# Optimization experiments

Hardware: AMD Instinct MI355X
Metric: run time of the kernel (lower is better)

The kernel has to match this reference:

```python
import jax, jax.numpy as jnp
import numpy as np

B, H, S, D = 2, 16, 2048, 64

def setup_inputs() -> dict:
    key = jax.random.key(0)
    kq, kk, kv, km = jax.random.split(key, 4)
    Q = jax.random.normal(kq, (B, H, S, D), dtype=jnp.float32)
    K = jax.random.normal(kk, (B, H, S, D), dtype=jnp.float32)
    V = jax.random.normal(kv, (B, H, S, D), dtype=jnp.float32)
    attn_mask = jax.random.bernoulli(km, 0.5, (B, H, S, S))  # True = masked
    return {"Q": Q, "K": K, "V": V, "attn_mask": attn_mask}

def reference(Q, K, V, attn_mask):
    eps = 1e-12
    d_tensor = K.shape[-1]
    # scores: [B, H, S, S]
    scores = jnp.einsum('bhqd,bhkd->bhqk', Q, K) / np.sqrt(d_tensor).astype(jnp.float32)
    # Faithful to source: first fill mask==0 positions with -eps, then mask==True with -1e9.
    scores = jnp.where(attn_mask == 0, jnp.float32(-eps), scores)
    scores = jnp.where(attn_mask, jnp.float32(-1e9), scores)
    attn = jax.nn.softmax(scores, axis=-1)
    context = jnp.einsum('bhqk,bhkd->bhqd', attn, V)
    # dropout=0.0 (eval) -> identity
    return (context, attn)
```

## Files before the change

kernel.cpp:

```cpp
#include <hip/hip_runtime.h>
#include <hip/hip_bf16.h>
#include <stdint.h>

#define S 2048
#define D 64
#define BH 32
#define NROWS (BH * S)
#define CTX_ELEMS (NROWS * D)
#define NVTB 512
#define VT_BYTES ((size_t)BH * 64 * 64 * 32 * 2)

typedef __attribute__((ext_vector_type(8))) __bf16 bf16x8;
typedef __attribute__((ext_vector_type(4))) float f32x4;
typedef __attribute__((ext_vector_type(4))) int   i32x4;


__global__ __launch_bounds__(256) void k_mask(const int* __restrict__ mask,
                                              const float* __restrict__ V,
                                              float* __restrict__ attn,
                                              uint32_t* __restrict__ packed,
                                              __bf16* __restrict__ VT,
                                              int use_vt) {
  const int t = threadIdx.x;

  if (blockIdx.x < NVTB) {
    if (!use_vt) return;
    const int bh = blockIdx.x >> 4;
    const int kk0 = (blockIdx.x & 15) * 4;
    const int c = t >> 2;
    const int g = t & 3;
#pragma unroll
    for (int s = 0; s < 4; ++s) {
      const int kk = kk0 + s;
      const float* vp = V + ((long)bh * S + kk * 32 + g * 8) * D + c;
      bf16x8 o;
#pragma unroll
      for (int j = 0; j < 8; ++j) o[j] = (__bf16)vp[(long)j * D];
      *reinterpret_cast<bf16x8*>(VT + (((long)bh * 64 + kk) * 64 + c) * 32 + g * 8) = o;
    }
    return;
  }

  const int r = blockIdx.x - NVTB;
  const long base = (long)r * S + t * 8;

  const i32x4 m0 = __builtin_nontemporal_load((const i32x4*)(mask + base));
  const i32x4 m1 = __builtin_nontemporal_load((const i32x4*)(mask + base + 4));
  int v[8] = {m0[0], m0[1], m0[2], m0[3], m1[0], m1[1], m1[2], m1[3]};

  unsigned byte = 0;
  int cnt = 0;
#pragma unroll
  for (int j = 0; j < 8; ++j) {
    unsigned u = (v[j] == 0) ? 1u : 0u;
    byte |= u << j;
    cnt += (int)u;
  }
#pragma unroll
  for (int off = 32; off > 0; off >>= 1) cnt += __shfl_down(cnt, off, 64);

  __shared__ int wsum[4];
  __shared__ unsigned char bts[256];
  bts[t] = (unsigned char)byte;
  if ((t & 63) == 0) wsum[t >> 6] = cnt;
  __syncthreads();

  const int total = wsum[0] + wsum[1] + wsum[2] + wsum[3];
  const float inv = (total > 0) ? (1.0f / (float)total) : 0.0f;

  f32x4 a0, a1;
  a0[0] = (byte & 1u)   ? inv : 0.0f;
  a0[1] = (byte & 2u)   ? inv : 0.0f;
  a0[2] = (byte & 4u)   ? inv : 0.0f;
  a0[3] = (byte & 8u)   ? inv : 0.0f;
  a1[0] = (byte & 16u)  ? inv : 0.0f;
  a1[1] = (byte & 32u)  ? inv : 0.0f;
  a1[2] = (byte & 64u)  ? inv : 0.0f;
  a1[3] = (byte & 128u) ? inv : 0.0f;
  __builtin_nontemporal_store(a0, (f32x4*)(attn + base));
  __builtin_nontemporal_store(a1, (f32x4*)(attn + base + 4));

  if (t < 64) {
    uint32_t w = (uint32_t)bts[4 * t]
               | ((uint32_t)bts[4 * t + 1] << 8)
               | ((uint32_t)bts[4 * t + 2] << 16)
               | ((uint32_t)bts[4 * t + 3] << 24);
    packed[(long)r * 64 + t] = w;
  }
}

#define BMC 128
template<bool USE_VT>
__global__ __launch_bounds__(128) void k_ctx(const uint32_t* __restrict__ packed,
                                             const float* __restrict__ V,
                                             const __bf16* __restrict__ VT,
                                             float* __restrict__ ctx) {
  const int flat = blockIdx.x;
  const int wid = (flat & 7) * ((NROWS / BMC) / 8) + (flat >> 3);
  const int qt = wid & 15;
  const int bh = wid >> 4;

  const int t = threadIdx.x;
  const int lane = t & 63;
  const int w = t >> 6;
  const int l15 = lane & 15;
  const int lk = lane >> 4;

  __shared__ uint32_t pk[BMC * 65];
  __shared__ float invs[BMC];

  const long R0 = (long)bh * S + (long)qt * BMC;

  for (int i = t; i < BMC * 64; i += 128)
    pk[(i >> 6) * 65 + (i & 63)] = packed[(R0 + (i >> 6)) * 64 + (i & 63)];
  __syncthreads();

  {
    int c = 0;
#pragma unroll
    for (int i = 0; i < 64; ++i) c += __popc(pk[t * 65 + i]);
    invs[t] = (c > 0) ? (1.0f / (float)c) : 0.0f;
  }
  __syncthreads();

  const uint8_t* pkb = (const uint8_t*)pk;
  const uint8_t* ap[4];
#pragma unroll
  for (int mt = 0; mt < 4; ++mt)
    ap[mt] = pkb + (w * 64 + mt * 16 + l15) * 260 + lk;
  const __bf16* vt0 = VT + ((long)bh * 64) * 64 * 32 + (long)l15 * 32 + lk * 8;
  const float* vf0 = V + (long)bh * S * D + (long)lk * 8 * D + l15;

  f32x4 acc[4][4];
#pragma unroll
  for (int a = 0; a < 4; ++a)
#pragma unroll
    for (int b = 0; b < 4; ++b) acc[a][b] = f32x4{0.f, 0.f, 0.f, 0.f};

  auto LOADB = [&](bf16x8* dst, uint32_t* by, int kk) {
    if (USE_VT) {
#pragma unroll
      for (int n4 = 0; n4 < 4; ++n4)
        dst[n4] = *reinterpret_cast<const bf16x8*>(vt0 + ((long)kk * 64 + n4 * 16) * 32);
    } else {
      const float* vp = vf0 + (long)kk * 32 * D;
#pragma unroll
      for (int n4 = 0; n4 < 4; ++n4) {
        bf16x8 x;
#pragma unroll
        for (int j = 0; j < 8; ++j) x[j] = (__bf16)vp[j * D + n4 * 16];
        dst[n4] = x;
      }
    }
#pragma unroll
    for (int mt = 0; mt < 4; ++mt) by[mt] = ap[mt][kk * 4];
  };

  auto COMPUTE = [&](const bf16x8* bf, const uint32_t* by) {
#pragma unroll
    for (int mt = 0; mt < 4; ++mt) {
      union { uint32_t u[4]; bf16x8 v; } am;
#pragma unroll
      for (int p = 0; p < 4; ++p) {
        am.u[p] = (((by[mt] >> (2 * p)) & 1u) ? 0x3F80u : 0u)
                | (((by[mt] >> (2 * p + 1)) & 1u) ? 0x3F800000u : 0u);
      }
#pragma unroll
      for (int n4 = 0; n4 < 4; ++n4)
        acc[mt][n4] = __builtin_amdgcn_mfma_f32_16x16x32_bf16(am.v, bf[n4], acc[mt][n4], 0, 0, 0);
    }
  };

  bf16x8 bA[4], bB[4];
  uint32_t byA[4], byB[4];
  LOADB(bA, byA, 0);
#pragma unroll 1
  for (int kk = 0; kk < S / 32; kk += 2) {
    LOADB(bB, byB, kk + 1);
    COMPUTE(bA, byA);
    if (kk + 2 < S / 32) LOADB(bA, byA, kk + 2);
    COMPUTE(bB, byB);
  }

#pragma unroll
  for (int mt = 0; mt < 4; ++mt) {
#pragma unroll
    for (int ri = 0; ri < 4; ++ri) {
      const int rloc = w * 64 + mt * 16 + lk * 4 + ri;
      const float iv = invs[rloc];
      const long orow = R0 + rloc;
#pragma unroll
      for (int n4 = 0; n4 < 4; ++n4)
        ctx[orow * D + n4 * 16 + l15] = acc[mt][n4][ri] * iv;
    }
  }
}

extern "C" void kernel_launch(void* const* d_in, const int* in_sizes, int n_in,
                              void* d_out, int out_size, void* d_ws, size_t ws_size,
                              hipStream_t stream) {
  (void)in_sizes; (void)n_in; (void)out_size;
  const float* V = (const float*)d_in[2];
  const int* mask = (const int*)d_in[3];
  float* ctx = (float*)d_out;
  float* attn = (float*)d_out + (size_t)CTX_ELEMS;
  uint32_t* packed = (uint32_t*)d_out;
  __bf16* VT = (__bf16*)d_ws;

  const int use_vt = (ws_size >= VT_BYTES) ? 1 : 0;
  k_mask<<<NVTB + NROWS, 256, 0, stream>>>(mask, V, attn, packed, VT, use_vt);
  if (use_vt)
    k_ctx<true><<<NROWS / BMC, 128, 0, stream>>>(packed, V, VT, ctx);
  else
    k_ctx<false><<<NROWS / BMC, 128, 0, stream>>>(packed, V, VT, ctx);
}
```

Baseline: 245.3 us.

## Use persistent wave-per-row mask kernel and smaller ctx query tiles

The mask kernel switches from one 256-thread block per row to a grid-stride loop with fixed block count, where each wave processes a whole row. Mask bits are packed via nibbles and cross-lane shuffles, so no shared memory or block barrier is needed. The context kernel halves its query tile from 128 to 64 rows, doubling the number of blocks to improve occupancy and load balance at the cost of more re-reads of V.

After: 233.5 us. 4.8% less time.

```diff
diff --git a/kernel.cpp b/kernel.cpp
--- a/kernel.cpp
+++ b/kernel.cpp
@@ -8,6 +8,7 @@
 #define NROWS (BH * S)
 #define CTX_ELEMS (NROWS * D)
 #define NVTB 512
+#define NSTB 2048
 #define VT_BYTES ((size_t)BH * 64 * 64 * 32 * 2)
 
 typedef __attribute__((ext_vector_type(8))) __bf16 bf16x8;
@@ -41,55 +42,53 @@
     return;
   }
 
-  const int r = blockIdx.x - NVTB;
-  const long base = (long)r * S + t * 8;
-
-  const i32x4 m0 = __builtin_nontemporal_load((const i32x4*)(mask + base));
-  const i32x4 m1 = __builtin_nontemporal_load((const i32x4*)(mask + base + 4));
-  int v[8] = {m0[0], m0[1], m0[2], m0[3], m1[0], m1[1], m1[2], m1[3]};
-
-  unsigned byte = 0;
-  int cnt = 0;
-#pragma unroll
-  for (int j = 0; j < 8; ++j) {
-    unsigned u = (v[j] == 0) ? 1u : 0u;
-    byte |= u << j;
-    cnt += (int)u;
-  }
-#pragma unroll
-  for (int off = 32; off > 0; off >>= 1) cnt += __shfl_down(cnt, off, 64);
-
-  __shared__ int wsum[4];
-  __shared__ unsigned char bts[256];
-  bts[t] = (unsigned char)byte;
-  if ((t & 63) == 0) wsum[t >> 6] = cnt;
-  __syncthreads();
-
-  const int total = wsum[0] + wsum[1] + wsum[2] + wsum[3];
-  const float inv = (total > 0) ? (1.0f / (float)total) : 0.0f;
-
-  f32x4 a0, a1;
-  a0[0] = (byte & 1u)   ? inv : 0.0f;
-  a0[1] = (byte & 2u)   ? inv : 0.0f;
-  a0[2] = (byte & 4u)   ? inv : 0.0f;
-  a0[3] = (byte & 8u)   ? inv : 0.0f;
-  a1[0] = (byte & 16u)  ? inv : 0.0f;
-  a1[1] = (byte & 32u)  ? inv : 0.0f;
-  a1[2] = (byte & 64u)  ? inv : 0.0f;
-  a1[3] = (byte & 128u) ? inv : 0.0f;
-  __builtin_nontemporal_store(a0, (f32x4*)(attn + base));
-  __builtin_nontemporal_store(a1, (f32x4*)(attn + base + 4));
-
-  if (t < 64) {
-    uint32_t w = (uint32_t)bts[4 * t]
-               | ((uint32_t)bts[4 * t + 1] << 8)
-               | ((uint32_t)bts[4 * t + 2] << 16)
-               | ((uint32_t)bts[4 * t + 3] << 24);
-    packed[(long)r * 64 + t] = w;
+  const int lane = t & 63;
+  const int W = (blockIdx.x - NVTB) * 4 + (t >> 6);
+
+#pragma unroll 1
+  for (int row = W; row < NROWS; row += NSTB * 4) {
+    const int* mrow = mask + (long)row * S;
+
+    uint32_t nib = 0;
+#pragma unroll
+    for (int j = 0; j < 8; ++j) {
+      const i32x4 m = __builtin_nontemporal_load(
+          (const i32x4*)(mrow + j * 256 + lane * 4));
+      nib |= (m[0] == 0 ? 1u : 0u) << (j * 4);
+      nib |= (m[1] == 0 ? 1u : 0u) << (j * 4 + 1);
+      nib |= (m[2] == 0 ? 1u : 0u) << (j * 4 + 2);
+      nib |= (m[3] == 0 ? 1u : 0u) << (j * 4 + 3);
+    }
+
+    int cnt = __popc(nib);
+#pragma unroll
+    for (int off = 1; off < 64; off <<= 1) cnt += __shfl_xor(cnt, off, 64);
+    const float inv = (cnt > 0) ? (1.0f / (float)cnt) : 0.0f;
+
+    float* arow = attn + (long)row * S;
+#pragma unroll
+    for (int j = 0; j < 8; ++j) {
+      f32x4 a;
+      a[0] = ((nib >> (j * 4)) & 1u)     ? inv : 0.0f;
+      a[1] = ((nib >> (j * 4 + 1)) & 1u) ? inv : 0.0f;
+      a[2] = ((nib >> (j * 4 + 2)) & 1u) ? inv : 0.0f;
+      a[3] = ((nib >> (j * 4 + 3)) & 1u) ? inv : 0.0f;
+      __builtin_nontemporal_store(a, (f32x4*)(arow + j * 256 + lane * 4));
+    }
+
+    uint32_t word = 0;
+    const int jsel = 4 * (lane >> 3);
+    const int lbase = (lane & 7) * 8;
+#pragma unroll
+    for (int d = 0; d < 8; ++d) {
+      const uint32_t nw = (uint32_t)__shfl((int)nib, lbase + d, 64);
+      word |= ((nw >> jsel) & 0xFu) << (4 * d);
+    }
+    packed[(long)row * 64 + lane] = word;
   }
 }
 
-#define BMC 128
+#define BMC 64
 template<bool USE_VT>
 __global__ __launch_bounds__(128) void k_ctx(const uint32_t* __restrict__ packed,
                                              const float* __restrict__ V,
@@ -97,8 +96,8 @@
                                              float* __restrict__ ctx) {
   const int flat = blockIdx.x;
   const int wid = (flat & 7) * ((NROWS / BMC) / 8) + (flat >> 3);
-  const int qt = wid & 15;
-  const int bh = wid >> 4;
+  const int qt = wid & 31;
+  const int bh = wid >> 5;
 
   const int t = threadIdx.x;
   const int lane = t & 63;
@@ -115,7 +114,7 @@
     pk[(i >> 6) * 65 + (i & 63)] = packed[(R0 + (i >> 6)) * 64 + (i & 63)];
   __syncthreads();
 
-  {
+  if (t < BMC) {
     int c = 0;
 #pragma unroll
     for (int i = 0; i < 64; ++i) c += __popc(pk[t * 65 + i]);
@@ -124,16 +123,16 @@
   __syncthreads();
 
   const uint8_t* pkb = (const uint8_t*)pk;
-  const uint8_t* ap[4];
-#pragma unroll
-  for (int mt = 0; mt < 4; ++mt)
-    ap[mt] = pkb + (w * 64 + mt * 16 + l15) * 260 + lk;
+  const uint8_t* ap[2];
+#pragma unroll
+  for (int mt = 0; mt < 2; ++mt)
+    ap[mt] = pkb + (w * 32 + mt * 16 + l15) * 260 + lk;
   const __bf16* vt0 = VT + ((long)bh * 64) * 64 * 32 + (long)l15 * 32 + lk * 8;
   const float* vf0 = V + (long)bh * S * D + (long)lk * 8 * D + l15;
 
-  f32x4 acc[4][4];
-#pragma unroll
-  for (int a = 0; a < 4; ++a)
+  f32x4 acc[2][4];
+#pragma unroll
+  for (int a = 0; a < 2; ++a)
 #pragma unroll
     for (int b = 0; b < 4; ++b) acc[a][b] = f32x4{0.f, 0.f, 0.f, 0.f};
 
@@ -153,12 +152,12 @@
       }
     }
 #pragma unroll
-    for (int mt = 0; mt < 4; ++mt) by[mt] = ap[mt][kk * 4];
+    for (int mt = 0; mt < 2; ++mt) by[mt] = ap[mt][kk * 4];
   };
 
   auto COMPUTE = [&](const bf16x8* bf, const uint32_t* by) {
 #pragma unroll
-    for (int mt = 0; mt < 4; ++mt) {
+    for (int mt = 0; mt < 2; ++mt) {
       union { uint32_t u[4]; bf16x8 v; } am;
 #pragma unroll
       for (int p = 0; p < 4; ++p) {
@@ -172,7 +171,7 @@
   };
 
   bf16x8 bA[4], bB[4];
-  uint32_t byA[4], byB[4];
+  uint32_t byA[2], byB[2];
   LOADB(bA, byA, 0);
 #pragma unroll 1
   for (int kk = 0; kk < S / 32; kk += 2) {
@@ -183,10 +182,10 @@
   }
 
 #pragma unroll
-  for (int mt = 0; mt < 4; ++mt) {
+  for (int mt = 0; mt < 2; ++mt) {
 #pragma unroll
     for (int ri = 0; ri < 4; ++ri) {
-      const int rloc = w * 64 + mt * 16 + lk * 4 + ri;
+      const int rloc = w * 32 + mt * 16 + lk * 4 + ri;
       const float iv = invs[rloc];
       const long orow = R0 + rloc;
 #pragma unroll
@@ -208,7 +207,7 @@
   __bf16* VT = (__bf16*)d_ws;
 
   const int use_vt = (ws_size >= VT_BYTES) ? 1 : 0;
-  k_mask<<<NVTB + NROWS, 256, 0, stream>>>(mask, V, attn, packed, VT, use_vt);
+  k_mask<<<NVTB + NSTB, 256, 0, stream>>>(mask, V, attn, packed, VT, use_vt);
   if (use_vt)
     k_ctx<true><<<NROWS / BMC, 128, 0, stream>>>(packed, V, VT, ctx);
   else
```
